# Performance work log

Measured on AMD Instinct MI355X. Metric: run time of the kernel, lower is better.

Reference implementation:

```python
import jax, jax.numpy as jnp
import numpy as np

T = 16  # fixed number of timesteps in the original module


def _lin(k, out_d, in_d):
    kw, kb = jax.random.split(k)
    s = 1.0 / np.sqrt(in_d)
    W = jax.random.uniform(kw, (out_d, in_d), minval=-s, maxval=s, dtype=jnp.float32)
    b = jax.random.uniform(kb, (out_d,), minval=-s, maxval=s, dtype=jnp.float32)
    return W, b


def setup_inputs() -> dict:
    key = jax.random.key(0)
    B = 8192
    k = jax.random.split(key, 16)
    x = jax.random.normal(k[0], (T, B, 64), dtype=jnp.float32)
    cue = jax.random.uniform(k[1], (B,), dtype=jnp.float32)
    hc1 = jnp.zeros((B, 256), jnp.float32)
    hc2 = jnp.zeros((B, 256), jnp.float32)
    hc3 = jnp.zeros((B, 256), jnp.float32)
    hc4 = jnp.zeros((B, 64), jnp.float32)
    W1i, b1i = _lin(k[2], 256, 64)
    W1h, b1h = _lin(k[3], 256, 256)
    Wf1, bf1 = _lin(k[4], 256, 64)
    W1o, b1o = _lin(k[5], 64, 256)
    W2i, b2i = _lin(k[6], 256, 64)
    W2h, b2h = _lin(k[7], 256, 256)
    Wf2, bf2 = _lin(k[8], 256, 64)
    W2o, b2o = _lin(k[9], 64, 256)
    W3i, b3i = _lin(k[10], 256, 130)
    W3h, b3h = _lin(k[11], 256, 256)
    W3o, b3o = _lin(k[12], 64, 256)
    Wfc, bfc = _lin(k[13], 2, 64)
    return dict(x=x, cue=cue, hc1=hc1, hc2=hc2, hc3=hc3, hc4=hc4,
                W1i=W1i, b1i=b1i, W1h=W1h, b1h=b1h, Wf1=Wf1, bf1=bf1, W1o=W1o, b1o=b1o,
                W2i=W2i, b2i=b2i, W2h=W2h, b2h=b2h, Wf2=Wf2, bf2=bf2, W2o=W2o, b2o=b2o,
                W3i=W3i, b3i=b3i, W3h=W3h, b3h=b3h, W3o=W3o, b3o=b3o, Wfc=Wfc, bfc=bfc)


def reference(x, cue, hc1, hc2, hc3, hc4,
              W1i, b1i, W1h, b1h, Wf1, bf1, W1o, b1o,
              W2i, b2i, W2h, b2h, Wf2, bf2, W2o, b2o,
              W3i, b3i, W3h, b3h, W3o, b3o, Wfc, bfc):
    B = x.shape[1]
    # cue row is the same at every timestep: [B, 2]
    cue_row = jnp.stack([cue * 10.0, 10.0 * jnp.abs(cue - 1.0)], axis=-1)

    def step(carry, xi):
        h1, h2, h3, h4 = carry
        # RNN stack 1 with feedback from hc4
        feed1 = h4 @ Wf1.T + bf1                                    # [B,256] (pre-tanh, stored)
        h1n = jnp.tanh(xi @ W1i.T + b1i + h1 @ W1h.T + b1h + jnp.tanh(feed1))
        out1 = jnp.tanh(h1n @ W1o.T + b1o)                           # [B,64]
        # RNN stack 2 with feedback from hc4
        feed2 = h4 @ Wf2.T + bf2
        h2n = jnp.tanh(xi @ W2i.T + b2i + h2 @ W2h.T + b2h + jnp.tanh(feed2))
        out2 = jnp.tanh(h2n @ W2o.T + b2o)                           # [B,64]
        # RNN stack 3 over concat(cue, out1, out2): [B,130]
        mid = jnp.concatenate([cue_row, out1, out2], axis=-1)
        h3n = jnp.tanh(mid @ W3i.T + b3i + h3 @ W3h.T + b3h)
        o = h3n @ W3o.T + b3o                                        # [B,64]; becomes next hc4
        of = jax.nn.relu(o)
        outf = of @ Wfc.T + bfc                                      # [B,2]
        return (h1n, h2n, h3n, o), (outf, out1, out2, feed1, feed2, of)

    (h1, h2, h3, h4), (oseq, o1, o2, f1, f2, ofa) = jax.lax.scan(
        step, (hc1, hc2, hc3, hc4), x)
    cue_arr = jnp.broadcast_to(cue_row[None, :, :], (T, B, 2))
    return (oseq, h1, h2, h3, h4, o1, o2, cue_arr, f1, f2, ofa)
```

## Files before the change

### kernel.cpp

```cpp
#include <hip/hip_runtime.h>

typedef unsigned short ushort_t;
typedef __attribute__((ext_vector_type(8))) __bf16 bf8v;
typedef __attribute__((ext_vector_type(4))) float f4v;
typedef __attribute__((ext_vector_type(4))) unsigned short us4v;

#define MFMA(a, b, c) __builtin_amdgcn_mfma_f32_16x16x32_bf16((a), (b), (c), 0, 0, 0)

#define B_TOT 8192
#define T_STEPS 16
#define M_TILE 32
#define LDH 264
#define LDS_SM 72
#define LDMID 168

#define OW1I 0
#define OW1H 16384
#define OWF1 81920
#define OW1O 98304
#define OW2I 114688
#define OW2H 131072
#define OWF2 196608
#define OW2O 212992
#define OW3I 229376
#define OW3H 270336
#define OW3O 335872
#define OWFC 352256
#define WS_TOTAL 353280

#define O_OSEQ 0
#define O_H1   262144
#define O_H2   2359296
#define O_H3   4456448
#define O_H4   6553600
#define O_O1   7077888
#define O_O2   15466496
#define O_CUE  23855104
#define O_F1   24117248
#define O_F2   57671680
#define O_OFA  91226112

__device__ __forceinline__ ushort_t f2bf(float f) {
  union { float f; unsigned u; } v; v.f = f;
  unsigned r = v.u + 0x7fffu + ((v.u >> 16) & 1u);
  return (ushort_t)(r >> 16);
}

__device__ __forceinline__ float fast_tanh(float x) {
  float e = __expf(2.0f * x);
  return 1.0f - 2.0f * __builtin_amdgcn_rcpf(e + 1.0f);
}

__device__ __forceinline__ void store_bf4(ushort_t* p, f4v v) {
  us4v q;
  q[0] = f2bf(v[0]); q[1] = f2bf(v[1]); q[2] = f2bf(v[2]); q[3] = f2bf(v[3]);
  *(us4v*)p = q;
}

__global__ void prep_kernel(const float* __restrict__ W1i, const float* __restrict__ W1h,
                            const float* __restrict__ Wf1, const float* __restrict__ W1o,
                            const float* __restrict__ W2i, const float* __restrict__ W2h,
                            const float* __restrict__ Wf2, const float* __restrict__ W2o,
                            const float* __restrict__ W3i, const float* __restrict__ W3h,
                            const float* __restrict__ W3o, const float* __restrict__ Wfc,
                            ushort_t* __restrict__ ws) {
  int i = blockIdx.x * blockDim.x + threadIdx.x;
  if (i >= WS_TOTAL) return;
  float v;
  if (i < OW1H)       v = W1i[i - OW1I];
  else if (i < OWF1)  v = W1h[i - OW1H];
  else if (i < OW1O)  v = Wf1[i - OWF1];
  else if (i < OW2I)  v = W1o[i - OW1O];
  else if (i < OW2H)  v = W2i[i - OW2I];
  else if (i < OWF2)  v = W2h[i - OW2H];
  else if (i < OW2O)  v = Wf2[i - OWF2];
  else if (i < OW3I)  v = W2o[i - OW2O];
  else if (i < OW3H) {
    int idx = i - OW3I; int j = idx / 160; int k = idx - j * 160;
    if (k < 64)       v = W3i[j * 130 + 2 + k];
    else if (k < 128) v = W3i[j * 130 + 66 + (k - 64)];
    else if (k < 130) v = W3i[j * 130 + (k - 128)];
    else              v = 0.0f;
  }
  else if (i < OW3O)  v = W3h[i - OW3H];
  else if (i < OWFC)  v = W3o[i - OW3O];
  else {
    int idx = i - OWFC; int j = idx / 64; int k = idx - j * 64;
    v = (j < 2) ? Wfc[j * 64 + k] : 0.0f;
  }
  ws[i] = f2bf(v);
}

__launch_bounds__(512)
__global__ void rnn_kernel(const float* __restrict__ x, const float* __restrict__ cue,
                           const float* __restrict__ hc1, const float* __restrict__ hc2,
                           const float* __restrict__ hc3, const float* __restrict__ hc4,
                           const float* __restrict__ b1i, const float* __restrict__ b1h,
                           const float* __restrict__ bf1p, const float* __restrict__ b1o,
                           const float* __restrict__ b2i, const float* __restrict__ b2h,
                           const float* __restrict__ bf2p, const float* __restrict__ b2o,
                           const float* __restrict__ b3i, const float* __restrict__ b3h,
                           const float* __restrict__ b3o, const float* __restrict__ bfc,
                           const ushort_t* __restrict__ ws, float* __restrict__ out) {
  __shared__ ushort_t hs1[M_TILE * LDH], hs2[M_TILE * LDH], hs3[M_TILE * LDH];
  __shared__ ushort_t h4s[M_TILE * LDS_SM], xs[M_TILE * LDS_SM], ofs[M_TILE * LDS_SM];
  __shared__ ushort_t mid[M_TILE * LDMID];

  const int tid  = threadIdx.x;
  const int m0   = blockIdx.x * M_TILE;
  const int lane = tid & 63;
  const int w    = tid >> 6;
  const int ln   = lane & 15;
  const int quad = lane >> 4;
  const int koff = quad * 8;
  const int jt0  = 2 * w;

  for (int i = tid; i < M_TILE * 256; i += 512) {
    int m = i >> 8, j = i & 255;
    hs1[m * LDH + j] = f2bf(hc1[(m0 + m) * 256 + j]);
    hs2[m * LDH + j] = f2bf(hc2[(m0 + m) * 256 + j]);
    hs3[m * LDH + j] = f2bf(hc3[(m0 + m) * 256 + j]);
  }
  for (int i = tid; i < M_TILE * 64; i += 512) {
    int m = i >> 6, j = i & 63;
    h4s[m * LDS_SM + j] = f2bf(hc4[(m0 + m) * 64 + j]);
  }
  for (int i = tid; i < M_TILE * LDMID; i += 512) mid[i] = 0;
  {
    int t = tid >> 5, r = tid & 31;
    float c = cue[m0 + r];
    float* oc = out + O_CUE + ((size_t)t * B_TOT + m0 + r) * 2;
    oc[0] = c * 10.0f;
    oc[1] = 10.0f * fabsf(c - 1.0f);
  }
  __syncthreads();
  if (tid < M_TILE) {
    float c = cue[m0 + tid];
    mid[tid * LDMID + 128] = f2bf(c * 10.0f);
    mid[tid * LDMID + 129] = f2bf(10.0f * fabsf(c - 1.0f));
  }

  f4v bf1v[2], bf2v[2], bih1v[2], bih2v[2], b3shv[2];
#pragma unroll
  for (int i = 0; i < 2; ++i) {
    int j0 = (jt0 + i) * 16 + quad * 4;
#pragma unroll
    for (int r = 0; r < 4; ++r) {
      bf1v[i][r]  = bf1p[j0 + r];
      bf2v[i][r]  = bf2p[j0 + r];
      bih1v[i][r] = b1i[j0 + r] + b1h[j0 + r];
      bih2v[i][r] = b2i[j0 + r] + b2h[j0 + r];
      b3shv[i][r] = b3i[j0 + r] + b3h[j0 + r];
    }
  }
  const int jto3 = w & 3;
  const int j0o3 = jto3 * 16 + quad * 4;
  const bool isOut2 = (w >= 4);
  f4v bo3v;
#pragma unroll
  for (int r = 0; r < 4; ++r) bo3v[r] = isOut2 ? b2o[j0o3 + r] : b1o[j0o3 + r];
  const int jto5 = w >> 1;
  const int j0o5 = jto5 * 16 + quad * 4;
  const int mo5  = (w & 1) * 16 + ln;
  f4v b3ov;
#pragma unroll
  for (int r = 0; r < 4; ++r) b3ov[r] = b3o[j0o5 + r];
  const float bfcv0 = bfc[0], bfcv1 = bfc[1];

  __syncthreads();

  f4v acc1[2][2], acc2[2][2], acc3[2][2];

  for (int t = 0; t < T_STEPS; ++t) {
    {
      int r = tid >> 4, c4 = (tid & 15) * 4;
      const float* xp = x + ((size_t)t * B_TOT + m0 + r) * 64 + c4;
      f4v xv = *(const f4v*)xp;
      store_bf4(&xs[r * LDS_SM + c4], xv);
    }
    {
      f4v aF1[2][2], aF2[2][2];
#pragma unroll
      for (int i = 0; i < 2; ++i) {
#pragma unroll
        for (int mt = 0; mt < 2; ++mt) { aF1[i][mt] = bf1v[i]; aF2[i][mt] = bf2v[i]; }
      }
#pragma unroll
      for (int kk = 0; kk < 64; kk += 32) {
        bf8v b0 = *(const bf8v*)&h4s[ln * LDS_SM + kk + koff];
        bf8v b1 = *(const bf8v*)&h4s[(16 + ln) * LDS_SM + kk + koff];
#pragma unroll
        for (int i = 0; i < 2; ++i) {
          const int ar = ((jt0 + i) * 16 + ln) * 64 + kk + koff;
          bf8v a1 = *(const bf8v*)&ws[OWF1 + ar];
          bf8v a2 = *(const bf8v*)&ws[OWF2 + ar];
          aF1[i][0] = MFMA(a1, b0, aF1[i][0]);
          aF1[i][1] = MFMA(a1, b1, aF1[i][1]);
          aF2[i][0] = MFMA(a2, b0, aF2[i][0]);
          aF2[i][1] = MFMA(a2, b1, aF2[i][1]);
        }
      }
#pragma unroll
      for (int i = 0; i < 2; ++i) {
#pragma unroll
        for (int mt = 0; mt < 2; ++mt) {
          int j0 = (jt0 + i) * 16 + quad * 4;
          int m  = mt * 16 + ln;
          size_t rowoff = ((size_t)t * B_TOT + m0 + m) * 256 + j0;
          *(f4v*)(out + O_F1 + rowoff) = aF1[i][mt];
          *(f4v*)(out + O_F2 + rowoff) = aF2[i][mt];
          f4v t1, t2;
#pragma unroll
          for (int r = 0; r < 4; ++r) {
            t1[r] = fast_tanh(aF1[i][mt][r]) + bih1v[i][r];
            t2[r] = fast_tanh(aF2[i][mt][r]) + bih2v[i][r];
          }
          acc1[i][mt] = t1; acc2[i][mt] = t2; acc3[i][mt] = b3shv[i];
        }
      }
    }
    __syncthreads();

#pragma unroll
    for (int kk = 0; kk < 64; kk += 32) {
      bf8v b0 = *(const bf8v*)&xs[ln * LDS_SM + kk + koff];
      bf8v b1 = *(const bf8v*)&xs[(16 + ln) * LDS_SM + kk + koff];
#pragma unroll
      for (int i = 0; i < 2; ++i) {
        const int ar = ((jt0 + i) * 16 + ln) * 64 + kk + koff;
        bf8v a1 = *(const bf8v*)&ws[OW1I + ar];
        bf8v a2 = *(const bf8v*)&ws[OW2I + ar];
        acc1[i][0] = MFMA(a1, b0, acc1[i][0]);
        acc1[i][1] = MFMA(a1, b1, acc1[i][1]);
        acc2[i][0] = MFMA(a2, b0, acc2[i][0]);
        acc2[i][1] = MFMA(a2, b1, acc2[i][1]);
      }
    }
#pragma unroll
    for (int kk = 0; kk < 256; kk += 32) {
      bf8v q1a = *(const bf8v*)&hs1[ln * LDH + kk + koff];
      bf8v q1b = *(const bf8v*)&hs1[(16 + ln) * LDH + kk + koff];
      bf8v q2a = *(const bf8v*)&hs2[ln * LDH + kk + koff];
      bf8v q2b = *(const bf8v*)&hs2[(16 + ln) * LDH + kk + koff];
      bf8v q3a = *(const bf8v*)&hs3[ln * LDH + kk + koff];
      bf8v q3b = *(const bf8v*)&hs3[(16 + ln) * LDH + kk + koff];
#pragma unroll
      for (int i = 0; i < 2; ++i) {
        const int ar = ((jt0 + i) * 16 + ln) * 256 + kk + koff;
        bf8v a1 = *(const bf8v*)&ws[OW1H + ar];
        bf8v a2 = *(const bf8v*)&ws[OW2H + ar];
        bf8v a3 = *(const bf8v*)&ws[OW3H + ar];
        acc1[i][0] = MFMA(a1, q1a, acc1[i][0]);
        acc1[i][1] = MFMA(a1, q1b, acc1[i][1]);
        acc2[i][0] = MFMA(a2, q2a, acc2[i][0]);
        acc2[i][1] = MFMA(a2, q2b, acc2[i][1]);
        acc3[i][0] = MFMA(a3, q3a, acc3[i][0]);
        acc3[i][1] = MFMA(a3, q3b, acc3[i][1]);
      }
    }
#pragma unroll
    for (int i = 0; i < 2; ++i) {
#pragma unroll
      for (int mt = 0; mt < 2; ++mt) {
#pragma unroll
        for (int r = 0; r < 4; ++r) {
          acc1[i][mt][r] = fast_tanh(acc1[i][mt][r]);
          acc2[i][mt][r] = fast_tanh(acc2[i][mt][r]);
        }
      }
    }
    if (t == T_STEPS - 1) {
#pragma unroll
      for (int i = 0; i < 2; ++i) {
#pragma unroll
        for (int mt = 0; mt < 2; ++mt) {
          int j0 = (jt0 + i) * 16 + quad * 4;
          int m  = mt * 16 + ln;
          *(f4v*)(out + O_H1 + (size_t)(m0 + m) * 256 + j0) = acc1[i][mt];
          *(f4v*)(out + O_H2 + (size_t)(m0 + m) * 256 + j0) = acc2[i][mt];
        }
      }
    }
    __syncthreads();

#pragma unroll
    for (int i = 0; i < 2; ++i) {
#pragma unroll
      for (int mt = 0; mt < 2; ++mt) {
        int j0 = (jt0 + i) * 16 + quad * 4;
        int m  = mt * 16 + ln;
        store_bf4(&hs1[m * LDH + j0], acc1[i][mt]);
        store_bf4(&hs2[m * LDH + j0], acc2[i][mt]);
      }
    }
    __syncthreads();

    {
      const ushort_t* hsrc = isOut2 ? hs2 : hs1;
      const int wbase = isOut2 ? OW2O : OW1O;
      f4v aO[2];
      aO[0] = bo3v; aO[1] = bo3v;
#pragma unroll
      for (int kk = 0; kk < 256; kk += 32) {
        bf8v b0 = *(const bf8v*)&hsrc[ln * LDH + kk + koff];
        bf8v b1 = *(const bf8v*)&hsrc[(16 + ln) * LDH + kk + koff];
        bf8v a  = *(const bf8v*)&ws[wbase + (jto3 * 16 + ln) * 256 + kk + koff];
        aO[0] = MFMA(a, b0, aO[0]);
        aO[1] = MFMA(a, b1, aO[1]);
      }
#pragma unroll
      for (int mt = 0; mt < 2; ++mt) {
#pragma unroll
        for (int r = 0; r < 4; ++r) aO[mt][r] = fast_tanh(aO[mt][r]);
        int m = mt * 16 + ln;
        size_t ob = ((size_t)t * B_TOT + m0 + m) * 64 + j0o3;
        *(f4v*)(out + (isOut2 ? O_O2 : O_O1) + ob) = aO[mt];
        store_bf4(&mid[m * LDMID + (isOut2 ? 64 : 0) + j0o3], aO[mt]);
      }
    }
    __syncthreads();

#pragma unroll
    for (int kk = 0; kk < 160; kk += 32) {
      bf8v b0 = *(const bf8v*)&mid[ln * LDMID + kk + koff];
      bf8v b1 = *(const bf8v*)&mid[(16 + ln) * LDMID + kk + koff];
#pragma unroll
      for (int i = 0; i < 2; ++i) {
        bf8v a = *(const bf8v*)&ws[OW3I + ((jt0 + i) * 16 + ln) * 160 + kk + koff];
        acc3[i][0] = MFMA(a, b0, acc3[i][0]);
        acc3[i][1] = MFMA(a, b1, acc3[i][1]);
      }
    }
#pragma unroll
    for (int i = 0; i < 2; ++i) {
#pragma unroll
      for (int mt = 0; mt < 2; ++mt) {
#pragma unroll
        for (int r = 0; r < 4; ++r) acc3[i][mt][r] = fast_tanh(acc3[i][mt][r]);
        int j0 = (jt0 + i) * 16 + quad * 4;
        int m  = mt * 16 + ln;
        if (t == T_STEPS - 1)
          *(f4v*)(out + O_H3 + (size_t)(m0 + m) * 256 + j0) = acc3[i][mt];
        store_bf4(&hs3[m * LDH + j0], acc3[i][mt]);
      }
    }
    __syncthreads();

    {
      f4v aO = b3ov;
#pragma unroll
      for (int kk = 0; kk < 256; kk += 32) {
        bf8v b = *(const bf8v*)&hs3[mo5 * LDH + kk + koff];
        bf8v a = *(const bf8v*)&ws[OW3O + (jto5 * 16 + ln) * 256 + kk + koff];
        aO = MFMA(a, b, aO);
      }
      store_bf4(&h4s[mo5 * LDS_SM + j0o5], aO);
      if (t == T_STEPS - 1)
        *(f4v*)(out + O_H4 + (size_t)(m0 + mo5) * 64 + j0o5) = aO;
      f4v rl;
#pragma unroll
      for (int r = 0; r < 4; ++r) rl[r] = fmaxf(aO[r], 0.0f);
      *(f4v*)(out + O_OFA + ((size_t)t * B_TOT + m0 + mo5) * 64 + j0o5) = rl;
      store_bf4(&ofs[mo5 * LDS_SM + j0o5], rl);
    }
    __syncthreads();

    if (w < 2) {
      f4v aFc;
      aFc[0] = (quad == 0) ? bfcv0 : 0.0f;
      aFc[1] = (quad == 0) ? bfcv1 : 0.0f;
      aFc[2] = 0.0f; aFc[3] = 0.0f;
#pragma unroll
      for (int kk = 0; kk < 64; kk += 32) {
        bf8v b = *(const bf8v*)&ofs[(w * 16 + ln) * LDS_SM + kk + koff];
        bf8v a = *(const bf8v*)&ws[OWFC + ln * 64 + kk + koff];
        aFc = MFMA(a, b, aFc);
      }
      if (quad == 0) {
        float* po = out + O_OSEQ + ((size_t)t * B_TOT + m0 + w * 16 + ln) * 2;
        po[0] = aFc[0];
        po[1] = aFc[1];
      }
    }
  }
}

extern "C" void kernel_launch(void* const* d_in, const int* in_sizes, int n_in,
                              void* d_out, int out_size, void* d_ws, size_t ws_size,
                              hipStream_t stream) {
  const float* x   = (const float*)d_in[0];
  const float* cue = (const float*)d_in[1];
  const float* hc1 = (const float*)d_in[2];
  const float* hc2 = (const float*)d_in[3];
  const float* hc3 = (const float*)d_in[4];
  const float* hc4 = (const float*)d_in[5];
  const float* W1i = (const float*)d_in[6];
  const float* b1i = (const float*)d_in[7];
  const float* W1h = (const float*)d_in[8];
  const float* b1h = (const float*)d_in[9];
  const float* Wf1 = (const float*)d_in[10];
  const float* bf1 = (const float*)d_in[11];
  const float* W1o = (const float*)d_in[12];
  const float* b1o = (const float*)d_in[13];
  const float* W2i = (const float*)d_in[14];
  const float* b2i = (const float*)d_in[15];
  const float* W2h = (const float*)d_in[16];
  const float* b2h = (const float*)d_in[17];
  const float* Wf2 = (const float*)d_in[18];
  const float* bf2 = (const float*)d_in[19];
  const float* W2o = (const float*)d_in[20];
  const float* b2o = (const float*)d_in[21];
  const float* W3i = (const float*)d_in[22];
  const float* b3i = (const float*)d_in[23];
  const float* W3h = (const float*)d_in[24];
  const float* b3h = (const float*)d_in[25];
  const float* W3o = (const float*)d_in[26];
  const float* b3o = (const float*)d_in[27];
  const float* Wfc = (const float*)d_in[28];
  const float* bfc = (const float*)d_in[29];

  ushort_t* ws = (ushort_t*)d_ws;
  float* out = (float*)d_out;

  prep_kernel<<<(WS_TOTAL + 511) / 512, 512, 0, stream>>>(
      W1i, W1h, Wf1, W1o, W2i, W2h, Wf2, W2o, W3i, W3h, W3o, Wfc, ws);

  rnn_kernel<<<B_TOT / M_TILE, 512, 0, stream>>>(
      x, cue, hc1, hc2, hc3, hc4,
      b1i, b1h, bf1, b1o, b2i, b2h, bf2, b2o, b3i, b3h, b3o, bfc,
      ws, out);
}
```

Baseline: 938.1 us.

## Halve batch tile to 16 rows, double-buffer hidden states, use nontemporal stores

```diff
diff --git a/kernel.cpp b/kernel.cpp
--- a/kernel.cpp
+++ b/kernel.cpp
@@ -9,7 +9,7 @@
 
 #define B_TOT 8192
 #define T_STEPS 16
-#define M_TILE 32
+#define M_TILE 16
 #define LDH 264
 #define LDS_SM 72
 #define LDMID 168
@@ -55,6 +55,10 @@
   us4v q;
   q[0] = f2bf(v[0]); q[1] = f2bf(v[1]); q[2] = f2bf(v[2]); q[3] = f2bf(v[3]);
   *(us4v*)p = q;
+}
+
+__device__ __forceinline__ void nt_store4(float* p, f4v v) {
+  __builtin_nontemporal_store(v, (f4v*)p);
 }
 
 __global__ void prep_kernel(const float* __restrict__ W1i, const float* __restrict__ W1h,
@@ -91,7 +95,7 @@
   ws[i] = f2bf(v);
 }
 
-__launch_bounds__(512)
+__launch_bounds__(512, 4)
 __global__ void rnn_kernel(const float* __restrict__ x, const float* __restrict__ cue,
                            const float* __restrict__ hc1, const float* __restrict__ hc2,
                            const float* __restrict__ hc3, const float* __restrict__ hc4,
@@ -102,7 +106,7 @@
                            const float* __restrict__ b3i, const float* __restrict__ b3h,
                            const float* __restrict__ b3o, const float* __restrict__ bfc,
                            const ushort_t* __restrict__ ws, float* __restrict__ out) {
-  __shared__ ushort_t hs1[M_TILE * LDH], hs2[M_TILE * LDH], hs3[M_TILE * LDH];
+  __shared__ ushort_t hs1[2][M_TILE * LDH], hs2[2][M_TILE * LDH], hs3[M_TILE * LDH];
   __shared__ ushort_t h4s[M_TILE * LDS_SM], xs[M_TILE * LDS_SM], ofs[M_TILE * LDS_SM];
   __shared__ ushort_t mid[M_TILE * LDMID];
 
@@ -117,17 +121,17 @@
 
   for (int i = tid; i < M_TILE * 256; i += 512) {
     int m = i >> 8, j = i & 255;
-    hs1[m * LDH + j] = f2bf(hc1[(m0 + m) * 256 + j]);
-    hs2[m * LDH + j] = f2bf(hc2[(m0 + m) * 256 + j]);
-    hs3[m * LDH + j] = f2bf(hc3[(m0 + m) * 256 + j]);
+    hs1[0][m * LDH + j] = f2bf(hc1[(m0 + m) * 256 + j]);
+    hs2[0][m * LDH + j] = f2bf(hc2[(m0 + m) * 256 + j]);
+    hs3[m * LDH + j]    = f2bf(hc3[(m0 + m) * 256 + j]);
   }
   for (int i = tid; i < M_TILE * 64; i += 512) {
     int m = i >> 6, j = i & 63;
     h4s[m * LDS_SM + j] = f2bf(hc4[(m0 + m) * 64 + j]);
   }
   for (int i = tid; i < M_TILE * LDMID; i += 512) mid[i] = 0;
-  {
-    int t = tid >> 5, r = tid & 31;
+  if (tid < 256) {
+    int t = tid >> 4, r = tid & 15;
     float c = cue[m0 + r];
     float* oc = out + O_CUE + ((size_t)t * B_TOT + m0 + r) * 2;
     oc[0] = c * 10.0f;
@@ -159,9 +163,7 @@
   f4v bo3v;
 #pragma unroll
   for (int r = 0; r < 4; ++r) bo3v[r] = isOut2 ? b2o[j0o3 + r] : b1o[j0o3 + r];
-  const int jto5 = w >> 1;
-  const int j0o5 = jto5 * 16 + quad * 4;
-  const int mo5  = (w & 1) * 16 + ln;
+  const int j0o5 = (w & 3) * 16 + quad * 4;
   f4v b3ov;
 #pragma unroll
   for (int r = 0; r < 4; ++r) b3ov[r] = b3o[j0o5 + r];
@@ -169,54 +171,46 @@
 
   __syncthreads();
 
-  f4v acc1[2][2], acc2[2][2], acc3[2][2];
+  f4v acc1[2], acc2[2], acc3[2];
 
   for (int t = 0; t < T_STEPS; ++t) {
-    {
+    const int cur = t & 1, nxt = cur ^ 1;
+
+    if (tid < 256) {
       int r = tid >> 4, c4 = (tid & 15) * 4;
       const float* xp = x + ((size_t)t * B_TOT + m0 + r) * 64 + c4;
       f4v xv = *(const f4v*)xp;
       store_bf4(&xs[r * LDS_SM + c4], xv);
     }
     {
-      f4v aF1[2][2], aF2[2][2];
-#pragma unroll
-      for (int i = 0; i < 2; ++i) {
-#pragma unroll
-        for (int mt = 0; mt < 2; ++mt) { aF1[i][mt] = bf1v[i]; aF2[i][mt] = bf2v[i]; }
-      }
+      f4v aF1[2], aF2[2];
+#pragma unroll
+      for (int i = 0; i < 2; ++i) { aF1[i] = bf1v[i]; aF2[i] = bf2v[i]; }
 #pragma unroll
       for (int kk = 0; kk < 64; kk += 32) {
         bf8v b0 = *(const bf8v*)&h4s[ln * LDS_SM + kk + koff];
-        bf8v b1 = *(const bf8v*)&h4s[(16 + ln) * LDS_SM + kk + koff];
 #pragma unroll
         for (int i = 0; i < 2; ++i) {
           const int ar = ((jt0 + i) * 16 + ln) * 64 + kk + koff;
           bf8v a1 = *(const bf8v*)&ws[OWF1 + ar];
           bf8v a2 = *(const bf8v*)&ws[OWF2 + ar];
-          aF1[i][0] = MFMA(a1, b0, aF1[i][0]);
-          aF1[i][1] = MFMA(a1, b1, aF1[i][1]);
-          aF2[i][0] = MFMA(a2, b0, aF2[i][0]);
-          aF2[i][1] = MFMA(a2, b1, aF2[i][1]);
+          aF1[i] = MFMA(a1, b0, aF1[i]);
+          aF2[i] = MFMA(a2, b0, aF2[i]);
         }
       }
 #pragma unroll
       for (int i = 0; i < 2; ++i) {
-#pragma unroll
-        for (int mt = 0; mt < 2; ++mt) {
-          int j0 = (jt0 + i) * 16 + quad * 4;
-          int m  = mt * 16 + ln;
-          size_t rowoff = ((size_t)t * B_TOT + m0 + m) * 256 + j0;
-          *(f4v*)(out + O_F1 + rowoff) = aF1[i][mt];
-          *(f4v*)(out + O_F2 + rowoff) = aF2[i][mt];
-          f4v t1, t2;
-#pragma unroll
-          for (int r = 0; r < 4; ++r) {
-            t1[r] = fast_tanh(aF1[i][mt][r]) + bih1v[i][r];
-            t2[r] = fast_tanh(aF2[i][mt][r]) + bih2v[i][r];
-          }
-          acc1[i][mt] = t1; acc2[i][mt] = t2; acc3[i][mt] = b3shv[i];
+        int j0 = (jt0 + i) * 16 + quad * 4;
+        size_t rowoff = ((size_t)t * B_TOT + m0 + ln) * 256 + j0;
+        nt_store4(out + O_F1 + rowoff, aF1[i]);
+        nt_store4(out + O_F2 + rowoff, aF2[i]);
+        f4v t1, t2;
+#pragma unroll
+        for (int r = 0; r < 4; ++r) {
+          t1[r] = fast_tanh(aF1[i][r]) + bih1v[i][r];
+          t2[r] = fast_tanh(aF2[i][r]) + bih2v[i][r];
         }
+        acc1[i] = t1; acc2[i] = t2; acc3[i] = b3shv[i];
       }
     }
     __syncthreads();
@@ -224,160 +218,118 @@
 #pragma unroll
     for (int kk = 0; kk < 64; kk += 32) {
       bf8v b0 = *(const bf8v*)&xs[ln * LDS_SM + kk + koff];
-      bf8v b1 = *(const bf8v*)&xs[(16 + ln) * LDS_SM + kk + koff];
 #pragma unroll
       for (int i = 0; i < 2; ++i) {
         const int ar = ((jt0 + i) * 16 + ln) * 64 + kk + koff;
         bf8v a1 = *(const bf8v*)&ws[OW1I + ar];
         bf8v a2 = *(const bf8v*)&ws[OW2I + ar];
-        acc1[i][0] = MFMA(a1, b0, acc1[i][0]);
-        acc1[i][1] = MFMA(a1, b1, acc1[i][1]);
-        acc2[i][0] = MFMA(a2, b0, acc2[i][0]);
-        acc2[i][1] = MFMA(a2, b1, acc2[i][1]);
+        acc1[i] = MFMA(a1, b0, acc1[i]);
+        acc2[i] = MFMA(a2, b0, acc2[i]);
       }
     }
 #pragma unroll
     for (int kk = 0; kk < 256; kk += 32) {
-      bf8v q1a = *(const bf8v*)&hs1[ln * LDH + kk + koff];
-      bf8v q1b = *(const bf8v*)&hs1[(16 + ln) * LDH + kk + koff];
-      bf8v q2a = *(const bf8v*)&hs2[ln * LDH + kk + koff];
-      bf8v q2b = *(const bf8v*)&hs2[(16 + ln) * LDH + kk + koff];
-      bf8v q3a = *(const bf8v*)&hs3[ln * LDH + kk + koff];
-      bf8v q3b = *(const bf8v*)&hs3[(16 + ln) * LDH + kk + koff];
+      bf8v q1 = *(const bf8v*)&hs1[cur][ln * LDH + kk + koff];
+      bf8v q2 = *(const bf8v*)&hs2[cur][ln * LDH + kk + koff];
+      bf8v q3 = *(const bf8v*)&hs3[ln * LDH + kk + koff];
 #pragma unroll
       for (int i = 0; i < 2; ++i) {
         const int ar = ((jt0 + i) * 16 + ln) * 256 + kk + koff;
         bf8v a1 = *(const bf8v*)&ws[OW1H + ar];
         bf8v a2 = *(const bf8v*)&ws[OW2H + ar];
         bf8v a3 = *(const bf8v*)&ws[OW3H + ar];
-        acc1[i][0] = MFMA(a1, q1a, acc1[i][0]);
-        acc1[i][1] = MFMA(a1, q1b, acc1[i][1]);
-        acc2[i][0] = MFMA(a2, q2a, acc2[i][0]);
-        acc2[i][1] = MFMA(a2, q2b, acc2[i][1]);
-        acc3[i][0] = MFMA(a3, q3a, acc3[i][0]);
-        acc3[i][1] = MFMA(a3, q3b, acc3[i][1]);
+        acc1[i] = MFMA(a1, q1, acc1[i]);
+        acc2[i] = MFMA(a2, q2, acc2[i]);
+        acc3[i] = MFMA(a3, q3, acc3[i]);
       }
     }
 #pragma unroll
     for (int i = 0; i < 2; ++i) {
 #pragma unroll
-      for (int mt = 0; mt < 2; ++mt) {
-#pragma unroll
-        for (int r = 0; r < 4; ++r) {
-          acc1[i][mt][r] = fast_tanh(acc1[i][mt][r]);
-          acc2[i][mt][r] = fast_tanh(acc2[i][mt][r]);
-        }
-      }
-    }
-    if (t == T_STEPS - 1) {
-#pragma unroll
-      for (int i = 0; i < 2; ++i) {
-#pragma unroll
-        for (int mt = 0; mt < 2; ++mt) {
-          int j0 = (jt0 + i) * 16 + quad * 4;
-          int m  = mt * 16 + ln;
-          *(f4v*)(out + O_H1 + (size_t)(m0 + m) * 256 + j0) = acc1[i][mt];
-          *(f4v*)(out + O_H2 + (size_t)(m0 + m) * 256 + j0) = acc2[i][mt];
-        }
-      }
-    }
-    __syncthreads();
-
-#pragma unroll
-    for (int i = 0; i < 2; ++i) {
-#pragma unroll
-      for (int mt = 0; mt < 2; ++mt) {
-        int j0 = (jt0 + i) * 16 + quad * 4;
-        int m  = mt * 16 + ln;
-        store_bf4(&hs1[m * LDH + j0], acc1[i][mt]);
-        store_bf4(&hs2[m * LDH + j0], acc2[i][mt]);
+      for (int r = 0; r < 4; ++r) {
+        acc1[i][r] = fast_tanh(acc1[i][r]);
+        acc2[i][r] = fast_tanh(acc2[i][r]);
+      }
+      int j0 = (jt0 + i) * 16 + quad * 4;
+      store_bf4(&hs1[nxt][ln * LDH + j0], acc1[i]);
+      store_bf4(&hs2[nxt][ln * LDH + j0], acc2[i]);
+      if (t == T_STEPS - 1) {
+        *(f4v*)(out + O_H1 + (size_t)(m0 + ln) * 256 + j0) = acc1[i];
+        *(f4v*)(out + O_H2 + (size_t)(m0 + ln) * 256 + j0) = acc2[i];
       }
     }
     __syncthreads();
 
     {
-      const ushort_t* hsrc = isOut2 ? hs2 : hs1;
+      const ushort_t* hsrc = isOut2 ? &hs2[nxt][0] : &hs1[nxt][0];
       const int wbase = isOut2 ? OW2O : OW1O;
-      f4v aO[2];
-      aO[0] = bo3v; aO[1] = bo3v;
+      f4v aO = bo3v;
 #pragma unroll
       for (int kk = 0; kk < 256; kk += 32) {
         bf8v b0 = *(const bf8v*)&hsrc[ln * LDH + kk + koff];
-        bf8v b1 = *(const bf8v*)&hsrc[(16 + ln) * LDH + kk + koff];
         bf8v a  = *(const bf8v*)&ws[wbase + (jto3 * 16 + ln) * 256 + kk + koff];
-        aO[0] = MFMA(a, b0, aO[0]);
-        aO[1] = MFMA(a, b1, aO[1]);
-      }
-#pragma unroll
-      for (int mt = 0; mt < 2; ++mt) {
-#pragma unroll
-        for (int r = 0; r < 4; ++r) aO[mt][r] = fast_tanh(aO[mt][r]);
-        int m = mt * 16 + ln;
-        size_t ob = ((size_t)t * B_TOT + m0 + m) * 64 + j0o3;
-        *(f4v*)(out + (isOut2 ? O_O2 : O_O1) + ob) = aO[mt];
-        store_bf4(&mid[m * LDMID + (isOut2 ? 64 : 0) + j0o3], aO[mt]);
-      }
+        aO = MFMA(a, b0, aO);
+      }
+#pragma unroll
+      for (int r = 0; r < 4; ++r) aO[r] = fast_tanh(aO[r]);
+      size_t ob = ((size_t)t * B_TOT + m0 + ln) * 64 + j0o3;
+      nt_store4(out + (isOut2 ? O_O2 : O_O1) + ob, aO);
+      store_bf4(&mid[ln * LDMID + (isOut2 ? 64 : 0) + j0o3], aO);
     }
     __syncthreads();
 
 #pragma unroll
     for (int kk = 0; kk < 160; kk += 32) {
       bf8v b0 = *(const bf8v*)&mid[ln * LDMID + kk + koff];
-      bf8v b1 = *(const bf8v*)&mid[(16 + ln) * LDMID + kk + koff];
 #pragma unroll
       for (int i = 0; i < 2; ++i) {
         bf8v a = *(const bf8v*)&ws[OW3I + ((jt0 + i) * 16 + ln) * 160 + kk + koff];
-        acc3[i][0] = MFMA(a, b0, acc3[i][0]);
-        acc3[i][1] = MFMA(a, b1, acc3[i][1]);
+        acc3[i] = MFMA(a, b0, acc3[i]);
       }
     }
 #pragma unroll
     for (int i = 0; i < 2; ++i) {
 #pragma unroll
-      for (int mt = 0; mt < 2; ++mt) {
-#pragma unroll
-        for (int r = 0; r < 4; ++r) acc3[i][mt][r] = fast_tanh(acc3[i][mt][r]);
-        int j0 = (jt0 + i) * 16 + quad * 4;
-        int m  = mt * 16 + ln;
-        if (t == T_STEPS - 1)
-          *(f4v*)(out + O_H3 + (size_t)(m0 + m) * 256 + j0) = acc3[i][mt];
-        store_bf4(&hs3[m * LDH + j0], acc3[i][mt]);
-      }
-    }
-    __syncthreads();
-
-    {
+      for (int r = 0; r < 4; ++r) acc3[i][r] = fast_tanh(acc3[i][r]);
+      int j0 = (jt0 + i) * 16 + quad * 4;
+      if (t == T_STEPS - 1)
+        *(f4v*)(out + O_H3 + (size_t)(m0 + ln) * 256 + j0) = acc3[i];
+      store_bf4(&hs3[ln * LDH + j0], acc3[i]);
+    }
+    __syncthreads();
+
+    if (w < 4) {
       f4v aO = b3ov;
 #pragma unroll
       for (int kk = 0; kk < 256; kk += 32) {
-        bf8v b = *(const bf8v*)&hs3[mo5 * LDH + kk + koff];
-        bf8v a = *(const bf8v*)&ws[OW3O + (jto5 * 16 + ln) * 256 + kk + koff];
+        bf8v b = *(const bf8v*)&hs3[ln * LDH + kk + koff];
+        bf8v a = *(const bf8v*)&ws[OW3O + ((w & 3) * 16 + ln) * 256 + kk + koff];
         aO = MFMA(a, b, aO);
       }
-      store_bf4(&h4s[mo5 * LDS_SM + j0o5], aO);
+      store_bf4(&h4s[ln * LDS_SM + j0o5], aO);
       if (t == T_STEPS - 1)
-        *(f4v*)(out + O_H4 + (size_t)(m0 + mo5) * 64 + j0o5) = aO;
+        *(f4v*)(out + O_H4 + (size_t)(m0 + ln) * 64 + j0o5) = aO;
       f4v rl;
 #pragma unroll
       for (int r = 0; r < 4; ++r) rl[r] = fmaxf(aO[r], 0.0f);
-      *(f4v*)(out + O_OFA + ((size_t)t * B_TOT + m0 + mo5) * 64 + j0o5) = rl;
-      store_bf4(&ofs[mo5 * LDS_SM + j0o5], rl);
-    }
-    __syncthreads();
-
-    if (w < 2) {
+      nt_store4(out + O_OFA + ((size_t)t * B_TOT + m0 + ln) * 64 + j0o5, rl);
+      store_bf4(&ofs[ln * LDS_SM + j0o5], rl);
+    }
+    __syncthreads();
+
+    if (w == 0) {
       f4v aFc;
       aFc[0] = (quad == 0) ? bfcv0 : 0.0f;
       aFc[1] = (quad == 0) ? bfcv1 : 0.0f;
       aFc[2] = 0.0f; aFc[3] = 0.0f;
 #pragma unroll
       for (int kk = 0; kk < 64; kk += 32) {
-        bf8v b = *(const bf8v*)&ofs[(w * 16 + ln) * LDS_SM + kk + koff];
+        bf8v b = *(const bf8v*)&ofs[ln * LDS_SM + kk + koff];
         bf8v a = *(const bf8v*)&ws[OWFC + ln * 64 + kk + koff];
         aFc = MFMA(a, b, aFc);
       }
       if (quad == 0) {
-        float* po = out + O_OSEQ + ((size_t)t * B_TOT + m0 + w * 16 + ln) * 2;
+        float* po = out + O_OSEQ + ((size_t)t * B_TOT + m0 + ln) * 2;
         po[0] = aFc[0];
         po[1] = aFc[1];
       }
```

After: 1.725 ms. 1.84x slower.
